# Kernel optimization log

Hardware: AMD Instinct MI355X
Metric: run time of the kernel (lower is better)

## Reference

```python
import jax, jax.numpy as jnp
import numpy as np

RADIUS = 3
OUT = 16
EPS = 1e-5


def setup_inputs() -> dict:
    key = jax.random.key(0)
    ks = jax.random.split(key, 20)
    N, E, EL, IN, OUT2 = 100000, 1600000, 6400000, 16, 2 * OUT
    inp = {
        "x": jax.random.normal(ks[0], (N, IN), jnp.float32),
        "y": jax.random.normal(ks[1], (E, IN), jnp.float32),
        "deg_g": jax.random.uniform(ks[2], (N, 1), jnp.float32),
        "deg_lg": jax.random.uniform(ks[3], (E, 1), jnp.float32),
        "theta_W": jax.random.normal(ks[4], (3 + RADIUS, OUT2, IN), jnp.float32) * 0.1,
        "theta_b": jax.random.normal(ks[5], (3 + RADIUS, OUT2), jnp.float32) * 0.1,
        "gamma_W": jax.random.normal(ks[6], (3 + RADIUS, OUT2, IN), jnp.float32) * 0.1,
        "gamma_b": jax.random.normal(ks[7], (3 + RADIUS, OUT2), jnp.float32) * 0.1,
        "bn_x_w": jnp.ones((OUT,), jnp.float32),
        "bn_x_b": jnp.zeros((OUT,), jnp.float32),
        "bn_y_w": jnp.ones((OUT,), jnp.float32),
        "bn_y_b": jnp.zeros((OUT,), jnp.float32),
        "src_g": jax.random.randint(ks[8], (E,), 0, N, jnp.int32),
        "dst_g": jax.random.randint(ks[9], (E,), 0, N, jnp.int32),
        "src_lg": jax.random.randint(ks[10], (EL,), 0, E, jnp.int32),
        "dst_lg": jax.random.randint(ks[11], (EL,), 0, E, jnp.int32),
        "eid2nid": jax.random.randint(ks[12], (E,), 0, N, jnp.int32),
    }
    return inp


def _spmm(z, src, dst, n):
    # copy_src + sum: out[v] = sum_{(u,v) in edges} z[u]
    return jax.ops.segment_sum(z[src], dst, num_segments=n)


def _aggregate(z, src, dst, n, radius):
    zl = []
    z = _spmm(z, src, dst, n)
    zl.append(z)
    for i in range(radius - 1):
        for _ in range(2 ** i):
            z = _spmm(z, src, dst, n)
        zl.append(z)
    return zl


def _lin(z, W, b):
    return z @ W.T + b


def _bn(h, w, b):
    m = h.mean(axis=0)
    v = h.var(axis=0)  # biased, as torch BN training normalization
    return (h - m) * jax.lax.rsqrt(v + EPS) * w + b


def reference(x, y, deg_g, deg_lg, theta_W, theta_b, gamma_W, gamma_b,
              bn_x_w, bn_x_b, bn_y_w, bn_y_b,
              src_g, dst_g, src_lg, dst_lg, eid2nid):
    N, E = x.shape[0], y.shape[0]
    # edge -> source-node feature gather (F.embedding)
    xy = x[eid2nid]
    # node branch
    x_list = [_lin(z, theta_W[3 + i], theta_b[3 + i])
              for i, z in enumerate(_aggregate(x, src_g, dst_g, N, RADIUS))]
    yx = jax.ops.segment_sum(y, dst_g, num_segments=N)  # copy_edge + sum
    xn = (_lin(x, theta_W[0], theta_b[0])
          + _lin(deg_g * x, theta_W[1], theta_b[1])
          + sum(x_list)
          + _lin(yx, theta_W[2], theta_b[2]))
    x_out = _bn(xn[:, :OUT] + jax.nn.relu(xn[:, OUT:]), bn_x_w, bn_x_b)
    # line-graph (edge) branch
    y_list = [_lin(z, gamma_W[3 + i], gamma_b[3 + i])
              for i, z in enumerate(_aggregate(y, src_lg, dst_lg, E, RADIUS))]
    xy_agg = _spmm(xy, src_lg, dst_lg, E)
    yn = (_lin(y, gamma_W[0], gamma_b[0])
          + _lin(deg_lg * y, gamma_W[1], gamma_b[1])
          + sum(y_list)
          + _lin(xy_agg, gamma_W[2], gamma_b[2]))
    y_out = _bn(yn[:, :OUT] + jax.nn.relu(yn[:, OUT:]), bn_y_w, bn_y_b)
    return (x_out, y_out)
```

## Files before the change

kernel.cpp:

```cpp
#include <hip/hip_runtime.h>
#include <stdint.h>

typedef __attribute__((ext_vector_type(8))) short bfx8;
typedef __attribute__((ext_vector_type(4))) float f32x4;

__device__ __forceinline__ float bf2f(unsigned short u){
  union { unsigned int i; float f; } x; x.i = ((unsigned int)u) << 16; return x.f;
}
__device__ __forceinline__ unsigned short f2bf(float f){
  union { float f; unsigned int i; } x; x.f = f;
  unsigned int r = x.i + 0x7fff + ((x.i >> 16) & 1);
  return (unsigned short)(r >> 16);
}
__device__ __forceinline__ void unpack8(uint4 v, float* o){
  o[0]=bf2f((unsigned short)(v.x)); o[1]=bf2f((unsigned short)(v.x>>16));
  o[2]=bf2f((unsigned short)(v.y)); o[3]=bf2f((unsigned short)(v.y>>16));
  o[4]=bf2f((unsigned short)(v.z)); o[5]=bf2f((unsigned short)(v.z>>16));
  o[6]=bf2f((unsigned short)(v.w)); o[7]=bf2f((unsigned short)(v.w>>16));
}
__device__ __forceinline__ uint4 pack8(const float* f){
  uint4 v;
  v.x = (unsigned)f2bf(f[0]) | ((unsigned)f2bf(f[1])<<16);
  v.y = (unsigned)f2bf(f[2]) | ((unsigned)f2bf(f[3])<<16);
  v.z = (unsigned)f2bf(f[4]) | ((unsigned)f2bf(f[5])<<16);
  v.w = (unsigned)f2bf(f[6]) | ((unsigned)f2bf(f[7])<<16);
  return v;
}
__device__ __forceinline__ void loadrow16_f32(const float* p, float* in){
  float4 a = *(const float4*)p;      float4 b = *(const float4*)(p+4);
  float4 c = *(const float4*)(p+8);  float4 d = *(const float4*)(p+12);
  in[0]=a.x; in[1]=a.y; in[2]=a.z; in[3]=a.w;
  in[4]=b.x; in[5]=b.y; in[6]=b.z; in[7]=b.w;
  in[8]=c.x; in[9]=c.y; in[10]=c.z; in[11]=c.w;
  in[12]=d.x; in[13]=d.y; in[14]=d.z; in[15]=d.w;
}
__device__ __forceinline__ bfx8 f32x8_to_bf(const float* p, float m){
  float4 a = *(const float4*)p; float4 b = *(const float4*)(p+4);
  bfx8 r;
  r[0]=(short)f2bf(a.x*m); r[1]=(short)f2bf(a.y*m); r[2]=(short)f2bf(a.z*m); r[3]=(short)f2bf(a.w*m);
  r[4]=(short)f2bf(b.x*m); r[5]=(short)f2bf(b.y*m); r[6]=(short)f2bf(b.z*m); r[7]=(short)f2bf(b.w*m);
  return r;
}

__global__ void k_f2b(const float* __restrict__ src, unsigned short* __restrict__ dst, long n8){
  long t = (long)blockIdx.x*blockDim.x + threadIdx.x;
  if (t >= n8) return;
  const float* p = src + t*8;
  float4 a = *(const float4*)p; float4 b = *(const float4*)(p+4);
  float f[8] = {a.x,a.y,a.z,a.w,b.x,b.y,b.z,b.w};
  *(uint4*)(dst + t*8) = pack8(f);
}

__global__ void __launch_bounds__(256) k_bcount(
    const int* __restrict__ dst, int n, int chunk, int shift, int nb,
    int* __restrict__ bkt_cnt){
  extern __shared__ int hist[];
  for (int b = threadIdx.x; b < nb; b += 256) hist[b] = 0;
  __syncthreads();
  int i0 = blockIdx.x * chunk;
  int iend = min(i0 + chunk, n);
  for (int i = i0 + threadIdx.x; i < iend; i += 256)
    atomicAdd(&hist[dst[i] >> shift], 1);
  __syncthreads();
  for (int b = threadIdx.x; b < nb; b += 256){
    int h = hist[b];
    if (h) atomicAdd(&bkt_cnt[b], h);
  }
}

__global__ void k_bscan(const int* __restrict__ bkt_cnt, int* __restrict__ bkt_base,
                        int* __restrict__ bcur, int nb){
  __shared__ int s[256];
  __shared__ int carry;
  if (threadIdx.x==0) carry = 0;
  __syncthreads();
  for (int base=0; base<nb; base+=256){
    int i = base + threadIdx.x;
    int v = (i<nb) ? bkt_cnt[i] : 0;
    s[threadIdx.x] = v; __syncthreads();
    for (int off=1; off<256; off<<=1){
      int t = (threadIdx.x>=off) ? s[threadIdx.x-off] : 0;
      __syncthreads();
      s[threadIdx.x] += t;
      __syncthreads();
    }
    int excl = s[threadIdx.x] - v + carry;
    if (i<nb){ bkt_base[i] = excl; bcur[i*16] = excl; }
    int tot = s[255];
    __syncthreads();
    if (threadIdx.x==0) carry += tot;
    __syncthreads();
  }
  if (threadIdx.x==0) bkt_base[nb] = carry;
}

template<int PAY>
__global__ void __launch_bounds__(256) k_scatter(
    const int* __restrict__ src, const int* __restrict__ dst, int n, int chunk,
    int shift, int nb, int* __restrict__ bcur, int* __restrict__ out){
  extern __shared__ int sh[];
  int* hist = sh;
  int* base = sh + nb;
  for (int b = threadIdx.x; b < nb; b += 256) hist[b] = 0;
  __syncthreads();
  int i0 = blockIdx.x * chunk;
  int iend = min(i0 + chunk, n);
  for (int i = i0 + threadIdx.x; i < iend; i += 256)
    atomicAdd(&hist[dst[i] >> shift], 1);
  __syncthreads();
  for (int b = threadIdx.x; b < nb; b += 256){
    int h = hist[b];
    base[b] = h ? atomicAdd(&bcur[b*16], h) : 0;
  }
  __syncthreads();
  for (int i = i0 + threadIdx.x; i < iend; i += 256){
    int d = dst[i];
    int b = d >> shift;
    int p = atomicAdd(&base[b], 1);
    if (PAY == 2) *(int2*)(out + (size_t)p*2) = make_int2(d, src[i]);
    else          *(int4*)(out + (size_t)p*4) = make_int4(d, src[i], i, 0);
  }
}

template<bool EID, int RLOG>
__global__ void __launch_bounds__(256) k_place2(
    const int* __restrict__ bkt_base, const int* __restrict__ binned,
    int nrows, int* __restrict__ rowptr,
    int* __restrict__ colA, int* __restrict__ colB){
  constexpr int R = 1 << RLOG;
  constexpr int K = R / 256;
  __shared__ int cnt[R];
  __shared__ int s[256];
  int rowBase = blockIdx.x << RLOG;
  int nr = min(R, nrows - rowBase);
  int beg = bkt_base[blockIdx.x], end = bkt_base[blockIdx.x+1];
  #pragma unroll
  for (int k=0;k<K;k++) cnt[threadIdx.x + k*256] = 0;
  __syncthreads();
  for (int i = beg + threadIdx.x; i < end; i += 256){
    int d = EID ? ((const int4*)binned)[i].x : ((const int2*)binned)[i].x;
    atomicAdd(&cnt[d & (R-1)], 1);
  }
  __syncthreads();
  int myBase = threadIdx.x * K;
  int part = 0;
  #pragma unroll
  for (int k=0;k<K;k++) part += cnt[myBase+k];
  s[threadIdx.x] = part; __syncthreads();
  for (int off=1; off<256; off<<=1){
    int t = (threadIdx.x>=off) ? s[threadIdx.x-off] : 0;
    __syncthreads();
    s[threadIdx.x] += t;
    __syncthreads();
  }
  int run = s[threadIdx.x] - part + beg;
  #pragma unroll
  for (int k=0;k<K;k++){
    int idx = myBase + k;
    int c = cnt[idx];
    cnt[idx] = run;
    if (idx < nr) rowptr[rowBase + idx] = run;
    run += c;
  }
  if (blockIdx.x == gridDim.x-1 && threadIdx.x == 255) rowptr[nrows] = end;
  __syncthreads();
  for (int i = beg + threadIdx.x; i < end; i += 256){
    if (EID){
      int4 v = ((const int4*)binned)[i];
      int p = atomicAdd(&cnt[v.x & (R-1)], 1);
      colA[p] = v.y; colB[p] = v.z;
    } else {
      int2 v = ((const int2*)binned)[i];
      int p = atomicAdd(&cnt[v.x & (R-1)], 1);
      colA[p] = v.y;
    }
  }
}

template<bool REMAP>
__global__ void __launch_bounds__(256) k_spmm(
    const int* __restrict__ rowptr, const int* __restrict__ col,
    const int* __restrict__ remap,
    const unsigned short* __restrict__ src, unsigned short* __restrict__ out, int nrows){
  int t = blockIdx.x*256 + threadIdx.x;
  int row = t >> 1, half = t & 1;
  if (row >= nrows) return;
  int beg = rowptr[row], end = rowptr[row+1];
  float acc[8] = {0,0,0,0,0,0,0,0};
  float acc2[8] = {0,0,0,0,0,0,0,0};
  const unsigned short* sp = src + (half<<3);
  int i = beg;
  for (; i+2 <= end; i += 2){
    int c0 = col[i], c1 = col[i+1];
    if (REMAP){ c0 = remap[c0]; c1 = remap[c1]; }
    uint4 v0 = *(const uint4*)(sp + ((size_t)c0<<4));
    uint4 v1 = *(const uint4*)(sp + ((size_t)c1<<4));
    float f0[8], f1[8]; unpack8(v0, f0); unpack8(v1, f1);
    #pragma unroll
    for (int j=0;j<8;j++){ acc[j] += f0[j]; acc2[j] += f1[j]; }
  }
  if (i < end){
    int c = col[i];
    if (REMAP) c = remap[c];
    uint4 v = *(const uint4*)(sp + ((size_t)c<<4));
    float f[8]; unpack8(v, f);
    #pragma unroll
    for (int j=0;j<8;j++) acc[j] += f[j];
  }
  #pragma unroll
  for (int j=0;j<8;j++) acc[j] += acc2[j];
  *(uint4*)(out + ((size_t)row<<4) + (half<<3)) = pack8(acc);
}

__global__ void __launch_bounds__(256) k_final_mfma(
    const float* __restrict__ base, const float* __restrict__ deg,
    const unsigned short* __restrict__ s2, const unsigned short* __restrict__ s3,
    const unsigned short* __restrict__ s4, const unsigned short* __restrict__ s5,
    const float* __restrict__ W, const float* __restrict__ Bb,
    float* __restrict__ hout, int nrows){
  int lane = threadIdx.x & 63;
  int l15 = lane & 15;
  int quad = lane >> 4;
  int kbase = quad * 8;
  int slocal = kbase >> 4;
  int k0 = kbase & 15;

  bfx8 bh[3][2], bl[3][2];
  #pragma unroll
  for (int kb=0; kb<3; ++kb){
    int s = kb*2 + slocal;
    #pragma unroll
    for (int t=0;t<2;++t){
      int o = t*16 + l15;
      const float* wp = W + s*512 + o*16 + k0;
      bfx8 hi, lo;
      #pragma unroll
      for (int j=0;j<8;j++){
        float w0 = wp[j];
        unsigned short h = f2bf(w0);
        unsigned short l2 = f2bf(w0 - bf2f(h));
        hi[j] = (short)h; lo[j] = (short)l2;
      }
      bh[kb][t] = hi; bl[kb][t] = lo;
    }
  }
  float bias0 = 0.f, bias1 = 0.f;
  #pragma unroll
  for (int s=0;s<6;s++){ bias0 += Bb[s*32 + l15]; bias1 += Bb[s*32 + 16 + l15]; }

  int ntiles = (nrows + 15) >> 4;
  int wstart = (blockIdx.x<<2) + (threadIdx.x>>6);
  int wstep  = gridDim.x<<2;
  for (int tile = wstart; tile < ntiles; tile += wstep){
    int R0 = tile << 4;
    int row = R0 + l15;
    int rowc = min(row, nrows-1);
    size_t ro = (size_t)rowc*16 + k0;
    float m = slocal ? deg[rowc] : 1.f;
    bfx8 a0 = f32x8_to_bf(base + ro, m);
    bfx8 a1 = *(const bfx8*)((slocal ? s3 : s2) + ro);
    bfx8 a2 = *(const bfx8*)((slocal ? s5 : s4) + ro);
    f32x4 c0 = {bias0,bias0,bias0,bias0};
    f32x4 c1 = {bias1,bias1,bias1,bias1};
    c0 = __builtin_amdgcn_mfma_f32_16x16x32_bf16(a0, bh[0][0], c0, 0,0,0);
    c1 = __builtin_amdgcn_mfma_f32_16x16x32_bf16(a0, bh[0][1], c1, 0,0,0);
    c0 = __builtin_amdgcn_mfma_f32_16x16x32_bf16(a1, bh[1][0], c0, 0,0,0);
    c1 = __builtin_amdgcn_mfma_f32_16x16x32_bf16(a1, bh[1][1], c1, 0,0,0);
    c0 = __builtin_amdgcn_mfma_f32_16x16x32_bf16(a2, bh[2][0], c0, 0,0,0);
    c1 = __builtin_amdgcn_mfma_f32_16x16x32_bf16(a2, bh[2][1], c1, 0,0,0);
    c0 = __builtin_amdgcn_mfma_f32_16x16x32_bf16(a0, bl[0][0], c0, 0,0,0);
    c1 = __builtin_amdgcn_mfma_f32_16x16x32_bf16(a0, bl[0][1], c1, 0,0,0);
    c0 = __builtin_amdgcn_mfma_f32_16x16x32_bf16(a1, bl[1][0], c0, 0,0,0);
    c1 = __builtin_amdgcn_mfma_f32_16x16x32_bf16(a1, bl[1][1], c1, 0,0,0);
    c0 = __builtin_amdgcn_mfma_f32_16x16x32_bf16(a2, bl[2][0], c0, 0,0,0);
    c1 = __builtin_amdgcn_mfma_f32_16x16x32_bf16(a2, bl[2][1], c1, 0,0,0);
    #pragma unroll
    for (int j=0;j<4;j++){
      int r = R0 + quad*4 + j;
      if (r < nrows) hout[(size_t)r*16 + l15] = c0[j] + fmaxf(c1[j], 0.f);
    }
  }
}

__global__ void __launch_bounds__(256) k_red(
    const float* __restrict__ h, int nrows, float* __restrict__ stats){
  __shared__ float redS[4][16];
  __shared__ float redQ[4][16];
  float ssum[16], ssq[16];
  #pragma unroll
  for (int c=0;c<16;c++){ ssum[c]=0.f; ssq[c]=0.f; }
  for (long r = (long)blockIdx.x*256 + threadIdx.x; r < nrows; r += (long)gridDim.x*256){
    float in[16];
    loadrow16_f32(h + r*16, in);
    #pragma unroll
    for (int c=0;c<16;c++){ ssum[c] += in[c]; ssq[c] += in[c]*in[c]; }
  }
  int lane = threadIdx.x & 63, wid = threadIdx.x >> 6;
  #pragma unroll
  for (int c=0;c<16;c++){
    float s = ssum[c], q = ssq[c];
    for (int off=32; off; off>>=1){ s += __shfl_xor(s, off, 64); q += __shfl_xor(q, off, 64); }
    if (lane==0){ redS[wid][c] = s; redQ[wid][c] = q; }
  }
  __syncthreads();
  if (threadIdx.x < 16){
    float s=0.f, q=0.f;
    #pragma unroll
    for (int w4=0; w4<4; w4++){ s += redS[w4][threadIdx.x]; q += redQ[w4][threadIdx.x]; }
    atomicAdd(&stats[threadIdx.x], s);
    atomicAdd(&stats[16 + threadIdx.x], q);
  }
}

__global__ void k_stats(const float* __restrict__ st,
                        const float* __restrict__ wx, const float* __restrict__ bx,
                        const float* __restrict__ wy, const float* __restrict__ by,
                        float* __restrict__ prm, int nx, int ny){
  int c = threadIdx.x;
  if (c < 16){
    float m  = st[c]/(float)nx;
    float v  = st[16+c]/(float)nx - m*m;
    float sc = wx[c] * rsqrtf(v + 1e-5f);
    prm[c] = sc; prm[16+c] = bx[c] - m*sc;
    float m2  = st[32+c]/(float)ny;
    float v2  = st[48+c]/(float)ny - m2*m2;
    float sc2 = wy[c] * rsqrtf(v2 + 1e-5f);
    prm[32+c] = sc2; prm[48+c] = by[c] - m2*sc2;
  }
}

__global__ void k_norm(float* __restrict__ out, const float* __restrict__ prm,
                       long nx, long ntot){
  long g = ((long)blockIdx.x*256 + threadIdx.x) * 8;
  if (g >= ntot) return;
  const float* p = (g < nx) ? prm : prm + 32;
  int cbase = (int)(g & 15);
  float4 a = *(float4*)(out + g);
  float4 b = *(float4*)(out + g + 4);
  float f[8] = {a.x,a.y,a.z,a.w,b.x,b.y,b.z,b.w};
  #pragma unroll
  for (int j=0;j<8;j++){ int c = cbase + j; f[j] = f[j]*p[c] + p[16+c]; }
  *(float4*)(out + g)     = make_float4(f[0],f[1],f[2],f[3]);
  *(float4*)(out + g + 4) = make_float4(f[4],f[5],f[6],f[7]);
}

extern "C" void kernel_launch(void* const* d_in, const int* in_sizes, int n_in,
                              void* d_out, int out_size, void* d_ws, size_t ws_size,
                              hipStream_t stream){
  const float* x      = (const float*)d_in[0];
  const float* y      = (const float*)d_in[1];
  const float* deg_g  = (const float*)d_in[2];
  const float* deg_lg = (const float*)d_in[3];
  const float* thW    = (const float*)d_in[4];
  const float* thB    = (const float*)d_in[5];
  const float* gaW    = (const float*)d_in[6];
  const float* gaB    = (const float*)d_in[7];
  const float* bnxw   = (const float*)d_in[8];
  const float* bnxb   = (const float*)d_in[9];
  const float* bnyw   = (const float*)d_in[10];
  const float* bnyb   = (const float*)d_in[11];
  const int* src_g   = (const int*)d_in[12];
  const int* dst_g   = (const int*)d_in[13];
  const int* src_lg  = (const int*)d_in[14];
  const int* dst_lg  = (const int*)d_in[15];
  const int* eid2nid = (const int*)d_in[16];

  const int N  = in_sizes[2];
  const int E  = in_sizes[3];
  const int EL = in_sizes[14];

  char* w = (char*)d_ws;
  auto alloc = [&](size_t bytes)->void*{
    void* p = (void*)w; w += (bytes + 255) & ~(size_t)255; return p;
  };
  int* g_rowptr   = (int*)alloc((size_t)(N+1)*4);
  int* g_col_src  = (int*)alloc((size_t)E*4);
  int* g_col_eid  = (int*)alloc((size_t)E*4);
  int* lg_rowptr  = (int*)alloc((size_t)(E+1)*4);
  int* lg_col     = (int*)alloc((size_t)EL*4);
  int* bcur       = (int*)alloc((size_t)1024*16*4);
  int* bkt_cnt_g  = (int*)alloc(1024*4);
  int* bkt_base_g = (int*)alloc(1025*4);
  int* bkt_cnt_l  = (int*)alloc(1024*4);
  int* bkt_base_l = (int*)alloc(1025*4);
  float* stats    = (float*)alloc(64*4);
  float* prm      = (float*)alloc(64*4);
  unsigned short* xb  = (unsigned short*)alloc((size_t)N*16*2);
  unsigned short* nz1 = (unsigned short*)alloc((size_t)N*16*2);
  unsigned short* nz2 = (unsigned short*)alloc((size_t)N*16*2);
  unsigned short* nz3 = (unsigned short*)alloc((size_t)N*16*2);
  unsigned short* nz4 = (unsigned short*)alloc((size_t)N*16*2);
  unsigned short* nyx = (unsigned short*)alloc((size_t)N*16*2);
  unsigned short* eb1 = (unsigned short*)alloc((size_t)E*16*2);
  unsigned short* eb2 = (unsigned short*)alloc((size_t)E*16*2);
  unsigned short* eb3 = (unsigned short*)alloc((size_t)E*16*2);
  unsigned short* yb  = (unsigned short*)alloc((size_t)E*16*2);
  unsigned short* eb4 = yb;
  int* binned_g = (int*)eb1;
  int* binned_l = (int*)eb2;

  hipMemsetAsync(bkt_cnt_g, 0, 1024*4, stream);
  hipMemsetAsync(bkt_cnt_l, 0, 1024*4, stream);
  hipMemsetAsync(stats, 0, 64*4, stream);

  long nx8 = (long)N*16/8, ny8 = (long)E*16/8;
  k_f2b<<<(int)((nx8+255)/256), 256, 0, stream>>>(x, xb, nx8);
  k_f2b<<<(int)((ny8+255)/256), 256, 0, stream>>>(y, yb, ny8);

  const int RLOG_G = 8;
  int nb_g = (N + (1<<RLOG_G) - 1) >> RLOG_G;
  k_bcount<<<(E+8191)/8192, 256, (size_t)nb_g*4, stream>>>(
      dst_g, E, 8192, RLOG_G, nb_g, bkt_cnt_g);
  k_bscan<<<1, 256, 0, stream>>>(bkt_cnt_g, bkt_base_g, bcur, nb_g);
  k_scatter<4><<<(E+8191)/8192, 256, (size_t)2*nb_g*4, stream>>>(
      src_g, dst_g, E, 8192, RLOG_G, nb_g, bcur, binned_g);
  k_place2<true, RLOG_G><<<nb_g, 256, 0, stream>>>(
      bkt_base_g, binned_g, N, g_rowptr, g_col_src, g_col_eid);

  const int RLOG_L = 11;
  int nb_l = (E + (1<<RLOG_L) - 1) >> RLOG_L;
  k_bcount<<<(EL+16383)/16384, 256, (size_t)nb_l*4, stream>>>(
      dst_lg, EL, 16384, RLOG_L, nb_l, bkt_cnt_l);
  k_bscan<<<1, 256, 0, stream>>>(bkt_cnt_l, bkt_base_l, bcur, nb_l);
  k_scatter<2><<<(EL+16383)/16384, 256, (size_t)2*nb_l*4, stream>>>(
      src_lg, dst_lg, EL, 16384, RLOG_L, nb_l, bcur, binned_l);
  k_place2<false, RLOG_L><<<nb_l, 256, 0, stream>>>(
      bkt_base_l, binned_l, E, lg_rowptr, lg_col, (int*)nullptr);

  int gs = (2*N+255)/256;
  int es = (2*E+255)/256;
  k_spmm<false><<<es, 256, 0, stream>>>(lg_rowptr, lg_col, nullptr, yb,  eb1, E);
  k_spmm<false><<<gs, 256, 0, stream>>>(g_rowptr, g_col_eid, nullptr, yb, nyx, N);
  k_spmm<false><<<gs, 256, 0, stream>>>(g_rowptr, g_col_src, nullptr, xb,  nz1, N);
  k_spmm<false><<<gs, 256, 0, stream>>>(g_rowptr, g_col_src, nullptr, nz1, nz2, N);
  k_spmm<false><<<gs, 256, 0, stream>>>(g_rowptr, g_col_src, nullptr, nz2, nz3, N);
  k_spmm<false><<<gs, 256, 0, stream>>>(g_rowptr, g_col_src, nullptr, nz3, nz4, N);
  k_spmm<false><<<es, 256, 0, stream>>>(lg_rowptr, lg_col, nullptr, eb1, eb2, E);
  k_spmm<false><<<es, 256, 0, stream>>>(lg_rowptr, lg_col, nullptr, eb2, eb3, E);
  k_spmm<false><<<es, 256, 0, stream>>>(lg_rowptr, lg_col, nullptr, eb3, eb4, E);
  k_spmm<true><<<es, 256, 0, stream>>>(lg_rowptr, lg_col, eid2nid, xb,  eb3, E);

  float* outp = (float*)d_out;
  int ntg = ((N + 15) >> 4, 0);
  (void)ntg;
  int tg = (N + 15) >> 4;  int bg2 = (tg + 3) / 4;  if (bg2 > 2048) bg2 = 2048;
  int te = (E + 15) >> 4;  int be2 = (te + 3) / 4;  if (be2 > 2048) be2 = 2048;
  k_final_mfma<<<bg2, 256, 0, stream>>>(x, deg_g, nyx, nz1, nz2, nz4,
                                        thW, thB, outp, N);
  k_final_mfma<<<be2, 256, 0, stream>>>(y, deg_lg, eb3, eb1, eb2, eb4,
                                        gaW, gaB, outp + (size_t)N*16, E);

  k_red<<<512, 256, 0, stream>>>(outp, N, stats);
  k_red<<<512, 256, 0, stream>>>(outp + (size_t)N*16, E, stats + 32);
  k_stats<<<1, 64, 0, stream>>>(stats, bnxw, bnxb, bnyw, bnyb, prm, N, E);
  long ntot = (long)(N + E) * 16;
  k_norm<<<(int)((ntot/8 + 255)/256), 256, 0, stream>>>(outp, prm, (long)N*16, ntot);
}
```

Baseline: 1.548 ms.

## Locally sort scatter chunks by bucket in LDS before writing binned edges

```diff
diff --git a/kernel.cpp b/kernel.cpp
--- a/kernel.cpp
+++ b/kernel.cpp
@@ -94,31 +94,58 @@
   if (threadIdx.x==0) bkt_base[nb] = carry;
 }
 
-template<int PAY>
-__global__ void __launch_bounds__(256) k_scatter(
-    const int* __restrict__ src, const int* __restrict__ dst, int n, int chunk,
+template<int PAY, int CHUNK, int NBMAX>
+__global__ void __launch_bounds__(256) k_scatter2(
+    const int* __restrict__ src, const int* __restrict__ dst, int n,
     int shift, int nb, int* __restrict__ bcur, int* __restrict__ out){
-  extern __shared__ int sh[];
-  int* hist = sh;
-  int* base = sh + nb;
+  __shared__ int hist[NBMAX];
+  __shared__ int delta[NBMAX];
+  __shared__ int s[256];
+  __shared__ int slot[CHUNK];
+  __shared__ int carry;
   for (int b = threadIdx.x; b < nb; b += 256) hist[b] = 0;
-  __syncthreads();
-  int i0 = blockIdx.x * chunk;
-  int iend = min(i0 + chunk, n);
+  if (threadIdx.x==0) carry = 0;
+  __syncthreads();
+  int i0 = blockIdx.x * CHUNK;
+  int iend = min(i0 + CHUNK, n);
   for (int i = i0 + threadIdx.x; i < iend; i += 256)
     atomicAdd(&hist[dst[i] >> shift], 1);
   __syncthreads();
-  for (int b = threadIdx.x; b < nb; b += 256){
-    int h = hist[b];
-    base[b] = h ? atomicAdd(&bcur[b*16], h) : 0;
-  }
-  __syncthreads();
+  for (int base = 0; base < nb; base += 256){
+    int b = base + threadIdx.x;
+    int v = (b < nb) ? hist[b] : 0;
+    s[threadIdx.x] = v; __syncthreads();
+    for (int off=1; off<256; off<<=1){
+      int t = (threadIdx.x>=off) ? s[threadIdx.x-off] : 0;
+      __syncthreads();
+      s[threadIdx.x] += t;
+      __syncthreads();
+    }
+    int excl = s[threadIdx.x] - v + carry;
+    int tot = s[255];
+    if (b < nb){
+      int g = v ? atomicAdd(&bcur[b*16], v) : 0;
+      delta[b] = g - excl;
+      hist[b] = excl;
+    }
+    __syncthreads();
+    if (threadIdx.x==0) carry += tot;
+    __syncthreads();
+  }
   for (int i = i0 + threadIdx.x; i < iend; i += 256){
+    int b = dst[i] >> shift;
+    int p = atomicAdd(&hist[b], 1);
+    slot[p] = i;
+  }
+  __syncthreads();
+  int cnt = iend - i0;
+  for (int j = threadIdx.x; j < cnt; j += 256){
+    int i = slot[j];
     int d = dst[i];
     int b = d >> shift;
-    int p = atomicAdd(&base[b], 1);
-    if (PAY == 2) *(int2*)(out + (size_t)p*2) = make_int2(d, src[i]);
-    else          *(int4*)(out + (size_t)p*4) = make_int4(d, src[i], i, 0);
+    int a = j + delta[b];
+    if (PAY == 2) *(int2*)(out + (size_t)a*2) = make_int2(d, src[i]);
+    else          *(int4*)(out + (size_t)a*4) = make_int4(d, src[i], i, 0);
   }
 }
 
@@ -412,8 +439,8 @@
   k_bcount<<<(E+8191)/8192, 256, (size_t)nb_g*4, stream>>>(
       dst_g, E, 8192, RLOG_G, nb_g, bkt_cnt_g);
   k_bscan<<<1, 256, 0, stream>>>(bkt_cnt_g, bkt_base_g, bcur, nb_g);
-  k_scatter<4><<<(E+8191)/8192, 256, (size_t)2*nb_g*4, stream>>>(
-      src_g, dst_g, E, 8192, RLOG_G, nb_g, bcur, binned_g);
+  k_scatter2<4, 4096, 512><<<(E+4095)/4096, 256, 0, stream>>>(
+      src_g, dst_g, E, RLOG_G, nb_g, bcur, binned_g);
   k_place2<true, RLOG_G><<<nb_g, 256, 0, stream>>>(
       bkt_base_g, binned_g, N, g_rowptr, g_col_src, g_col_eid);
 
@@ -422,8 +449,8 @@
   k_bcount<<<(EL+16383)/16384, 256, (size_t)nb_l*4, stream>>>(
       dst_lg, EL, 16384, RLOG_L, nb_l, bkt_cnt_l);
   k_bscan<<<1, 256, 0, stream>>>(bkt_cnt_l, bkt_base_l, bcur, nb_l);
-  k_scatter<2><<<(EL+16383)/16384, 256, (size_t)2*nb_l*4, stream>>>(
-      src_lg, dst_lg, EL, 16384, RLOG_L, nb_l, bcur, binned_l);
+  k_scatter2<2, 16384, 1024><<<(EL+16383)/16384, 256, 0, stream>>>(
+      src_lg, dst_lg, EL, RLOG_L, nb_l, bcur, binned_l);
   k_place2<false, RLOG_L><<<nb_l, 256, 0, stream>>>(
       bkt_base_l, binned_l, E, lg_rowptr, lg_col, (int*)nullptr);
 
@@ -441,8 +468,6 @@
   k_spmm<true><<<es, 256, 0, stream>>>(lg_rowptr, lg_col, eid2nid, xb,  eb3, E);
 
   float* outp = (float*)d_out;
-  int ntg = ((N + 15) >> 4, 0);
-  (void)ntg;
   int tg = (N + 15) >> 4;  int bg2 = (tg + 3) / 4;  if (bg2 > 2048) bg2 = 2048;
   int te = (E + 15) >> 4;  int be2 = (te + 3) / 4;  if (be2 > 2048) be2 = 2048;
   k_final_mfma<<<bg2, 256, 0, stream>>>(x, deg_g, nyx, nz1, nz2, nz4,
```

New measurement: 1.571 ms. No clear change (+1.5%).
